# Optimization experiments

Measured on AMD Instinct MI355X. Metric: run time of the kernel, lower is better.

The kernel has to match this reference:

```python
import jax, jax.numpy as jnp
import numpy as np

N_NODES = 100000
N_EDGES = 3200000
NEG_SLOPE = 0.2  # PyG GATConv default
EPS = 1e-16      # PyG softmax denominator guard


def setup_inputs() -> dict:
    key = jax.random.key(0)
    ks = jax.random.split(key, 12)
    x = jax.random.normal(ks[0], (N_NODES, 4), dtype=jnp.float32)
    edge_index = jax.random.randint(ks[1], (2, N_EDGES), 0, N_NODES, dtype=jnp.int32)
    # conv1: in=4, heads=4, out=16, concat -> 64
    W1 = jax.random.normal(ks[2], (4, 64), dtype=jnp.float32) * 0.5
    a_src1 = jax.random.normal(ks[3], (4, 16), dtype=jnp.float32) * 0.3
    a_dst1 = jax.random.normal(ks[4], (4, 16), dtype=jnp.float32) * 0.3
    b1 = jnp.zeros((64,), dtype=jnp.float32)
    # conv2: in=64, heads=1, out=2, no concat
    W2 = jax.random.normal(ks[5], (64, 2), dtype=jnp.float32) * 0.2
    a_src2 = jax.random.normal(ks[6], (1, 2), dtype=jnp.float32) * 0.3
    a_dst2 = jax.random.normal(ks[7], (1, 2), dtype=jnp.float32) * 0.3
    b2 = jnp.zeros((2,), dtype=jnp.float32)
    return dict(x=x, edge_index=edge_index, W1=W1, a_src1=a_src1, a_dst1=a_dst1,
                b1=b1, W2=W2, a_src2=a_src2, a_dst2=a_dst2, b2=b2)


def _gat_layer(h_in, src, dst, W, a_s, a_d, b, heads, out_dim, concat):
    n = h_in.shape[0]
    h = (h_in @ W).reshape(n, heads, out_dim)            # [N, H, F]
    alpha_s = jnp.einsum('nhf,hf->nh', h, a_s)           # [N, H]
    alpha_d = jnp.einsum('nhf,hf->nh', h, a_d)
    e = jax.nn.leaky_relu(alpha_s[src] + alpha_d[dst], NEG_SLOPE)  # [E, H]
    # segment softmax over incoming edges of each dst node
    m = jax.ops.segment_max(e, dst, num_segments=n)      # [N, H]
    e = jnp.exp(e - m[dst])
    s = jax.ops.segment_sum(e, dst, num_segments=n)
    alpha = e / (s[dst] + EPS)                            # [E, H]
    msg = h[src] * alpha[:, :, None]                      # [E, H, F]
    out = jax.ops.segment_sum(msg, dst, num_segments=n)   # [N, H, F]
    if concat:
        out = out.reshape(n, heads * out_dim)
    else:
        out = out.mean(axis=1)
    return out + b


def reference(x, edge_index, W1, a_src1, a_dst1, b1, W2, a_src2, a_dst2, b2):
    n = x.shape[0]
    loop = jnp.arange(n, dtype=edge_index.dtype)
    src = jnp.concatenate([edge_index[0], loop])  # PyG add_self_loops=True
    dst = jnp.concatenate([edge_index[1], loop])
    h = jax.nn.elu(_gat_layer(x, src, dst, W1, a_src1, a_dst1, b1, 4, 16, True))
    h = _gat_layer(h, src, dst, W2, a_src2, a_dst2, b2, 1, 2, False)
    return jax.nn.log_softmax(h, axis=1)
```

## Files before the change

### kernel.cpp

```cpp
#include <hip/hip_runtime.h>
#include <hip/hip_fp16.h>
#include <math.h>

#define NEG_SLOPE 0.2f
#define EPS_F 1e-16f

#define P1_NB 256
#define P1S_THREADS 1024
#define LOCAL_BITS 7
#define NLOCAL 128
#define MAX_BEDGES 5632
#define REGS_PB 6
#define SCAN_SHIFT 11

__device__ __forceinline__ float leaky(float v) {
    return fmaxf(v, NEG_SLOPE * v);
}

__global__ void k_p1hist(const int* __restrict__ dst, int* __restrict__ histT,
                         int E, int chunk, int nbucket) {
    __shared__ int cnt[1024];
    int blk = blockIdx.x, t = threadIdx.x;
    for (int i = t; i < nbucket; i += P1S_THREADS) cnt[i] = 0;
    __syncthreads();
    int s = blk * chunk, e = min(E, s + chunk);
    for (int i = s + t; i < e; i += P1S_THREADS)
        atomicAdd(&cnt[dst[i] >> LOCAL_BITS], 1);
    __syncthreads();
    for (int i = t; i < nbucket; i += P1S_THREADS)
        histT[i * P1_NB + blk] = cnt[i];
}

__global__ void k_scan1(const int* __restrict__ in, int* __restrict__ out,
                        int* __restrict__ blockSums, int M) {
    __shared__ int sdata[256];
    int t = threadIdx.x;
    int base = blockIdx.x * 2048 + t * 8;
    int v[8];
    int total = 0;
#pragma unroll
    for (int k = 0; k < 8; ++k) {
        int idx = base + k;
        v[k] = (idx < M) ? in[idx] : 0;
        total += v[k];
    }
    sdata[t] = total;
    __syncthreads();
    for (int off = 1; off < 256; off <<= 1) {
        int x = (t >= off) ? sdata[t - off] : 0;
        __syncthreads();
        sdata[t] += x;
        __syncthreads();
    }
    int run = sdata[t] - total;
#pragma unroll
    for (int k = 0; k < 8; ++k) {
        int idx = base + k;
        if (idx < M) out[idx] = run;
        run += v[k];
    }
    if (t == 255) blockSums[blockIdx.x] = sdata[255];
}

__global__ void k_scan2(int* __restrict__ bs, int n) {
    __shared__ int s[128];
    int t = threadIdx.x;
    int v = (t < n) ? bs[t] : 0;
    s[t] = v;
    __syncthreads();
    for (int o = 1; o < 128; o <<= 1) {
        int x = (t >= o) ? s[t - o] : 0;
        __syncthreads();
        s[t] += x;
        __syncthreads();
    }
    if (t < n) bs[t] = s[t] - v;
}

__global__ void __launch_bounds__(1024)
k_scatterA(const int* __restrict__ src, const int* __restrict__ dst,
           const int* __restrict__ baseT, const int* __restrict__ bsScan,
           unsigned int* __restrict__ packed, int E, int chunk, int nbucket,
           const float* __restrict__ x, const float* __restrict__ W1,
           const float* __restrict__ a_src1, const float* __restrict__ a_dst1,
           __half* __restrict__ h1h, float* __restrict__ as1,
           float* __restrict__ ad1, int N) {
    __shared__ int cnt[1024];
    int blk = blockIdx.x, t = threadIdx.x;
    if (blk < P1_NB) {
        for (int i = t; i < nbucket; i += P1S_THREADS) {
            int idx = i * P1_NB + blk;
            cnt[i] = baseT[idx] + bsScan[idx >> SCAN_SHIFT];
        }
        __syncthreads();
        int s = blk * chunk, e = min(E, s + chunk);
        for (int i = s + t; i < e; i += P1S_THREADS) {
            int d = dst[i];
            int pos = atomicAdd(&cnt[d >> LOCAL_BITS], 1);
            packed[pos] = ((unsigned int)(d & (NLOCAL - 1)) << 23) | (unsigned int)src[i];
        }
    } else {
        int node = (blk - P1_NB) * 16 + (t >> 6);
        if (node >= N) return;
        int lane = t & 63;
        float4 xv = ((const float4*)x)[node];
        float h = xv.x * W1[lane] + xv.y * W1[64 + lane] +
                  xv.z * W1[128 + lane] + xv.w * W1[192 + lane];
        h1h[(size_t)node * 64 + lane] = __float2half(h);
        float as = h * a_src1[lane];
        float ad = h * a_dst1[lane];
#pragma unroll
        for (int m = 8; m >= 1; m >>= 1) {
            as += __shfl_xor(as, m, 16);
            ad += __shfl_xor(ad, m, 16);
        }
        if ((lane & 15) == 0) {
            int head = lane >> 4;
            as1[node * 4 + head] = as;
            ad1[node * 4 + head] = ad;
        }
    }
}

__global__ void k_fineL1(const unsigned int* __restrict__ packed, const int* __restrict__ baseT,
                         const int* __restrict__ bsScan,
                         const __half* __restrict__ h1h, const float* __restrict__ as1,
                         const float* __restrict__ ad1, const float* __restrict__ b1,
                         const float* __restrict__ W2, const float* __restrict__ a_src2,
                         const float* __restrict__ a_dst2,
                         int* __restrict__ csr, int* __restrict__ rowptr,
                         uint2* __restrict__ node2, int N, int E) {
    __shared__ int cnt[NLOCAL];
    __shared__ int off[NLOCAL];
    __shared__ int cur[NLOCAL];
    __shared__ unsigned int eb[MAX_BEDGES];

    int b = blockIdx.x, t = threadIdx.x;
    int nbucket = gridDim.x;
    int nodeBase = b << LOCAL_BITS;

    int i0 = b * P1_NB;
    int startE = baseT[i0] + bsScan[i0 >> SCAN_SHIFT];
    int endE = E;
    if (b != nbucket - 1) {
        int i1 = (b + 1) * P1_NB;
        endE = baseT[i1] + bsScan[i1 >> SCAN_SHIFT];
    }
    int ne = endE - startE;
    if (ne > MAX_BEDGES) ne = MAX_BEDGES;

    if (t < NLOCAL) cnt[t] = 0;
    __syncthreads();

    unsigned int pk[REGS_PB];
#pragma unroll
    for (int k = 0; k < REGS_PB; ++k) {
        int i = t + k * 1024;
        pk[k] = (i < ne) ? packed[startE + i] : 0xFFFFFFFFu;
    }
#pragma unroll
    for (int k = 0; k < REGS_PB; ++k)
        if (pk[k] != 0xFFFFFFFFu) atomicAdd(&cnt[pk[k] >> 23], 1);
    __syncthreads();
    if (t < NLOCAL) cur[t] = cnt[t];
    __syncthreads();
    for (int o = 1; o < NLOCAL; o <<= 1) {
        int v = (t < NLOCAL && t >= o) ? cur[t - o] : 0;
        __syncthreads();
        if (t < NLOCAL) cur[t] += v;
        __syncthreads();
    }
    if (t < NLOCAL) {
        int excl = cur[t] - cnt[t];
        off[t] = excl;
        int node = nodeBase + t;
        if (node < N) rowptr[node] = startE + excl;
    }
    if (b == 0 && t == 0) rowptr[N] = E;
    __syncthreads();
    if (t < NLOCAL) cur[t] = off[t];
    __syncthreads();
#pragma unroll
    for (int k = 0; k < REGS_PB; ++k)
        if (pk[k] != 0xFFFFFFFFu) {
            int pos = atomicAdd(&cur[pk[k] >> 23], 1);
            eb[pos] = pk[k];
        }
    __syncthreads();
    for (int i = t; i < ne; i += 1024)
        csr[startE + i] = (int)(eb[i] & 0x7FFFFFu);

    int wave = t >> 6;
    int lane = t & 63;
    int head4 = lane & 3;
    int j     = lane >> 2;
    int sub   = lane >> 4;
    int fl    = lane & 15;
    int h     = fl >> 2;

    for (int q = 0; q < 8; ++q) {
        int local = wave * 8 + q;
        int node = nodeBase + local;
        if (node >= N) break;
        int beg = off[local];
        int end = beg + cnt[local];

        float ad_s1 = ad1[node * 4 + head4];
        float pself4 = __expf(leaky(as1[node * 4 + head4] + ad_s1));
        float psum = (lane < 4) ? pself4 : 0.f;

        float pselfF = __shfl(pself4, h);
        float a0 = 0.f, a1 = 0.f, a2 = 0.f, a3 = 0.f;
        if (sub == 0) {
            float2 raw = *(const float2*)(h1h + ((size_t)node << 6) + (fl << 2));
            __half2 h01 = *reinterpret_cast<__half2*>(&raw.x);
            __half2 h23 = *reinterpret_cast<__half2*>(&raw.y);
            float2 f01 = __half22float2(h01), f23 = __half22float2(h23);
            a0 = pselfF * f01.x; a1 = pselfF * f01.y;
            a2 = pselfF * f23.x; a3 = pselfF * f23.y;
        }

        for (int c = beg; c < end; c += 16) {
            int e = c + j;
            bool valid = e < end;
            int s = (int)(eb[valid ? e : beg] & 0x7FFFFFu);
            float v = leaky(as1[s * 4 + head4] + ad_s1);
            float p = valid ? __expf(v) : 0.f;
            psum += p;

            int s_q[4];
#pragma unroll
            for (int m = 0; m < 4; ++m) s_q[m] = __shfl(s, m * 16 + sub * 4);
            float2 raw[4];
#pragma unroll
            for (int m = 0; m < 4; ++m)
                raw[m] = *(const float2*)(h1h + ((size_t)s_q[m] << 6) + (fl << 2));
            float p_q[4];
#pragma unroll
            for (int m = 0; m < 4; ++m) p_q[m] = __shfl(p, m * 16 + sub * 4 + h);
#pragma unroll
            for (int m = 0; m < 4; ++m) {
                __half2 h01 = *reinterpret_cast<__half2*>(&raw[m].x);
                __half2 h23 = *reinterpret_cast<__half2*>(&raw[m].y);
                float2 f01 = __half22float2(h01), f23 = __half22float2(h23);
                a0 = fmaf(p_q[m], f01.x, a0);
                a1 = fmaf(p_q[m], f01.y, a1);
                a2 = fmaf(p_q[m], f23.x, a2);
                a3 = fmaf(p_q[m], f23.y, a3);
            }
        }

        a0 += __shfl_xor(a0, 16); a0 += __shfl_xor(a0, 32);
        a1 += __shfl_xor(a1, 16); a1 += __shfl_xor(a1, 32);
        a2 += __shfl_xor(a2, 16); a2 += __shfl_xor(a2, 32);
        a3 += __shfl_xor(a3, 16); a3 += __shfl_xor(a3, 32);

#pragma unroll
        for (int m = 4; m <= 32; m <<= 1) psum += __shfl_xor(psum, m);
        float psumF = __shfl(psum, h);
        float inv = 1.f / (psumF + EPS_F);

        float4 b1v = ((const float4*)b1)[fl];
        float o0 = a0 * inv + b1v.x;
        float o1 = a1 * inv + b1v.y;
        float o2 = a2 * inv + b1v.z;
        float o3 = a3 * inv + b1v.w;
        float e0 = o0 > 0.f ? o0 : (__expf(o0) - 1.f);
        float e1 = o1 > 0.f ? o1 : (__expf(o1) - 1.f);
        float e2 = o2 > 0.f ? o2 : (__expf(o2) - 1.f);
        float e3 = o3 > 0.f ? o3 : (__expf(o3) - 1.f);

        float4 w01 = ((const float4*)W2)[fl * 2];
        float4 w23 = ((const float4*)W2)[fl * 2 + 1];
        float c0 = e0 * w01.x + e1 * w01.z + e2 * w23.x + e3 * w23.z;
        float c1 = e0 * w01.y + e1 * w01.w + e2 * w23.y + e3 * w23.w;
#pragma unroll
        for (int m = 8; m >= 1; m >>= 1) {
            c0 += __shfl_xor(c0, m);
            c1 += __shfl_xor(c1, m);
        }
        if (lane == 0) {
            float as2 = c0 * a_src2[0] + c1 * a_src2[1];
            float ad2 = c0 * a_dst2[0] + c1 * a_dst2[1];
            __half2 hc = __floats2half2_rn(c0, c1);
            __half2 ha = __floats2half2_rn(as2, ad2);
            node2[node] = make_uint2(*(unsigned int*)&hc, *(unsigned int*)&ha);
        }
    }
}

__global__ void k_layer2(const int* __restrict__ rowptr, const int* __restrict__ csr,
                         const uint2* __restrict__ node2, const float* __restrict__ b2,
                         float* __restrict__ out, int N) {
    int node = blockIdx.x * 16 + (threadIdx.x >> 4);
    if (node >= N) return;
    int sl = threadIdx.x & 15;

    uint2 mraw = node2[node];
    __half2 mch = *reinterpret_cast<__half2*>(&mraw.x);
    __half2 mah = *reinterpret_cast<__half2*>(&mraw.y);
    float2 mc = __half22float2(mch);
    float2 ma = __half22float2(mah);
    float ad = ma.y;
    int beg = rowptr[node], end = rowptr[node + 1];

    float psum = 0.f, a0 = 0.f, a1 = 0.f;
    for (int e = beg + sl; e < end; e += 16) {
        uint2 sraw = node2[csr[e]];
        __half2 sch = *reinterpret_cast<__half2*>(&sraw.x);
        __half2 sah = *reinterpret_cast<__half2*>(&sraw.y);
        float2 sc = __half22float2(sch);
        float2 sa = __half22float2(sah);
        float p = __expf(leaky(sa.x + ad));
        psum += p;
        a0 = fmaf(p, sc.x, a0);
        a1 = fmaf(p, sc.y, a1);
    }
    if (sl == 0) {
        float p = __expf(leaky(ma.x + ad));
        psum += p;
        a0 = fmaf(p, mc.x, a0);
        a1 = fmaf(p, mc.y, a1);
    }
#pragma unroll
    for (int m = 8; m >= 1; m >>= 1) {
        psum += __shfl_xor(psum, m);
        a0 += __shfl_xor(a0, m);
        a1 += __shfl_xor(a1, m);
    }
    if (sl == 0) {
        float inv = 1.f / (psum + EPS_F);
        float o0 = a0 * inv + b2[0];
        float o1 = a1 * inv + b2[1];
        float mx = fmaxf(o0, o1);
        float lse = mx + logf(__expf(o0 - mx) + __expf(o1 - mx));
        out[node * 2 + 0] = o0 - lse;
        out[node * 2 + 1] = o1 - lse;
    }
}


extern "C" void kernel_launch(void* const* d_in, const int* in_sizes, int n_in,
                              void* d_out, int out_size, void* d_ws, size_t ws_size,
                              hipStream_t stream) {
    const float* x      = (const float*)d_in[0];
    const int*   ei     = (const int*)d_in[1];
    const float* W1     = (const float*)d_in[2];
    const float* a_src1 = (const float*)d_in[3];
    const float* a_dst1 = (const float*)d_in[4];
    const float* b1     = (const float*)d_in[5];
    const float* W2     = (const float*)d_in[6];
    const float* a_src2 = (const float*)d_in[7];
    const float* a_dst2 = (const float*)d_in[8];
    const float* b2     = (const float*)d_in[9];
    float* out = (float*)d_out;

    int N = in_sizes[0] / 4;
    int E = in_sizes[1] / 2;
    const int* e_src = ei;
    const int* e_dst = ei + E;

    int nbucket = (N + NLOCAL - 1) >> LOCAL_BITS;
    int M = nbucket * P1_NB;

    char* w = (char*)d_ws;
    auto alloc = [&](size_t bytes) -> void* {
        void* p = (void*)w;
        w += (bytes + 255) & ~(size_t)255;
        return p;
    };
    __half* h1h       = (__half*)alloc((size_t)N * 64 * 2);
    float*  as1       = (float*)alloc((size_t)N * 4 * 4);
    float*  ad1       = (float*)alloc((size_t)N * 4 * 4);
    uint2*  node2     = (uint2*)alloc((size_t)N * 8);
    int*    rowptr    = (int*)alloc((size_t)(N + 1) * 4);
    int*    histT     = (int*)alloc((size_t)M * 4);
    int*    baseT     = (int*)alloc((size_t)M * 4);
    int*    blockSums = (int*)alloc(256 * 4);
    int*    csr       = (int*)alloc((size_t)E * 4);
    unsigned int* packed = (unsigned int*)alloc((size_t)E * 4);

    int chunk = (E + P1_NB - 1) / P1_NB;
    int nbScan = (M + 2047) / 2048;
    int nodeb16 = (N + 15) / 16;

    k_p1hist<<<P1_NB, P1S_THREADS, 0, stream>>>(e_dst, histT, E, chunk, nbucket);
    k_scan1<<<nbScan, 256, 0, stream>>>(histT, baseT, blockSums, M);
    k_scan2<<<1, 128, 0, stream>>>(blockSums, nbScan);
    k_scatterA<<<P1_NB + nodeb16, P1S_THREADS, 0, stream>>>(
        e_src, e_dst, baseT, blockSums, packed, E, chunk, nbucket,
        x, W1, a_src1, a_dst1, h1h, as1, ad1, N);
    k_fineL1<<<nbucket, 1024, 0, stream>>>(packed, baseT, blockSums,
                                           h1h, as1, ad1, b1, W2,
                                           a_src2, a_dst2, csr, rowptr, node2, N, E);
    k_layer2<<<nodeb16, 256, 0, stream>>>(rowptr, csr, node2, b2, out, N);
}
```

Before: 241.1 us.

## Fuse histogram, scan and scatter into one persistent kernel with grid barriers

Replaces the histogram, two-level scan and scatter kernels with a single 256-block kernel. It keeps each block's dst chunk in registers, accumulates per-bucket counts with global atomics, and synchronises the grid with atomic spin barriers. Block 0 then scans the bucket totals, and each block claims its offsets atomically before scattering the packed edges. Layer-1 node projection is folded in between the passes. This removes several launches and the reload of dst. In exchange, edge order within a bucket becomes nondeterministic, and the code relies on all 256 blocks being co-resident for the spin barrier to avoid deadlock.

```diff
diff --git a/kernel.cpp b/kernel.cpp
--- a/kernel.cpp
+++ b/kernel.cpp
@@ -5,125 +5,121 @@
 #define NEG_SLOPE 0.2f
 #define EPS_F 1e-16f
 
-#define P1_NB 256
-#define P1S_THREADS 1024
 #define LOCAL_BITS 7
 #define NLOCAL 128
 #define MAX_BEDGES 5632
 #define REGS_PB 6
-#define SCAN_SHIFT 11
+#define BUILD_NB 256
+#define DREGS 13
 
 __device__ __forceinline__ float leaky(float v) {
     return fmaxf(v, NEG_SLOPE * v);
 }
 
-__global__ void k_p1hist(const int* __restrict__ dst, int* __restrict__ histT,
-                         int E, int chunk, int nbucket) {
+__global__ void __launch_bounds__(1024, 4)
+k_build(const int* __restrict__ src, const int* __restrict__ dst,
+        int* __restrict__ ctrs, int* __restrict__ bucketBase, int* __restrict__ bucketCur,
+        unsigned int* __restrict__ packed, int E, int chunk, int nbucket,
+        const float* __restrict__ x, const float* __restrict__ W1,
+        const float* __restrict__ a_src1, const float* __restrict__ a_dst1,
+        __half* __restrict__ h1h, float* __restrict__ as1,
+        float* __restrict__ ad1, int N) {
     __shared__ int cnt[1024];
+    __shared__ int lcur[1024];
+
     int blk = blockIdx.x, t = threadIdx.x;
-    for (int i = t; i < nbucket; i += P1S_THREADS) cnt[i] = 0;
-    __syncthreads();
-    int s = blk * chunk, e = min(E, s + chunk);
-    for (int i = s + t; i < e; i += P1S_THREADS)
-        atomicAdd(&cnt[dst[i] >> LOCAL_BITS], 1);
-    __syncthreads();
-    for (int i = t; i < nbucket; i += P1S_THREADS)
-        histT[i * P1_NB + blk] = cnt[i];
-}
-
-__global__ void k_scan1(const int* __restrict__ in, int* __restrict__ out,
-                        int* __restrict__ blockSums, int M) {
-    __shared__ int sdata[256];
-    int t = threadIdx.x;
-    int base = blockIdx.x * 2048 + t * 8;
-    int v[8];
-    int total = 0;
-#pragma unroll
-    for (int k = 0; k < 8; ++k) {
-        int idx = base + k;
-        v[k] = (idx < M) ? in[idx] : 0;
-        total += v[k];
-    }
-    sdata[t] = total;
-    __syncthreads();
-    for (int off = 1; off < 256; off <<= 1) {
-        int x = (t >= off) ? sdata[t - off] : 0;
+    int* bucketCnt = ctrs;
+    int* barA = ctrs + 1024;
+    int* barB = ctrs + 1025;
+
+    cnt[t] = 0;
+    __syncthreads();
+
+    int s0 = blk * chunk, e0 = min(E, s0 + chunk);
+    int dreg[DREGS];
+#pragma unroll
+    for (int k = 0; k < DREGS; ++k) {
+        int i = s0 + t + k * 1024;
+        dreg[k] = (i < e0) ? dst[i] : -1;
+    }
+#pragma unroll
+    for (int k = 0; k < DREGS; ++k)
+        if (dreg[k] >= 0) atomicAdd(&cnt[dreg[k] >> LOCAL_BITS], 1);
+    __syncthreads();
+    if (t < nbucket && cnt[t] > 0) atomicAdd(&bucketCnt[t], cnt[t]);
+
+    {
+        int nspb = (N + BUILD_NB - 1) / BUILD_NB;
+        int base = blk * nspb, lim = min(N, base + nspb);
+        int lane = t & 63;
+        for (int node = base + (t >> 6); node < lim; node += 16) {
+            float4 xv = ((const float4*)x)[node];
+            float h = xv.x * W1[lane] + xv.y * W1[64 + lane] +
+                      xv.z * W1[128 + lane] + xv.w * W1[192 + lane];
+            h1h[(size_t)node * 64 + lane] = __float2half(h);
+            float as = h * a_src1[lane];
+            float ad = h * a_dst1[lane];
+#pragma unroll
+            for (int m = 8; m >= 1; m >>= 1) {
+                as += __shfl_xor(as, m, 16);
+                ad += __shfl_xor(ad, m, 16);
+            }
+            if ((lane & 15) == 0) {
+                as1[node * 4 + (lane >> 4)] = as;
+                ad1[node * 4 + (lane >> 4)] = ad;
+            }
+        }
+    }
+
+    __threadfence();
+    __syncthreads();
+    if (t == 0) {
+        atomicAdd(barA, 1);
+        while (atomicAdd(barA, 0) < (int)gridDim.x) __builtin_amdgcn_s_sleep(8);
+    }
+    __syncthreads();
+    __threadfence();
+
+    if (blk == 0) {
+        int v = (t < nbucket) ? bucketCnt[t] : 0;
+        lcur[t] = v;
         __syncthreads();
-        sdata[t] += x;
-        __syncthreads();
-    }
-    int run = sdata[t] - total;
-#pragma unroll
-    for (int k = 0; k < 8; ++k) {
-        int idx = base + k;
-        if (idx < M) out[idx] = run;
-        run += v[k];
-    }
-    if (t == 255) blockSums[blockIdx.x] = sdata[255];
-}
-
-__global__ void k_scan2(int* __restrict__ bs, int n) {
-    __shared__ int s[128];
-    int t = threadIdx.x;
-    int v = (t < n) ? bs[t] : 0;
-    s[t] = v;
-    __syncthreads();
-    for (int o = 1; o < 128; o <<= 1) {
-        int x = (t >= o) ? s[t - o] : 0;
-        __syncthreads();
-        s[t] += x;
-        __syncthreads();
-    }
-    if (t < n) bs[t] = s[t] - v;
-}
-
-__global__ void __launch_bounds__(1024)
-k_scatterA(const int* __restrict__ src, const int* __restrict__ dst,
-           const int* __restrict__ baseT, const int* __restrict__ bsScan,
-           unsigned int* __restrict__ packed, int E, int chunk, int nbucket,
-           const float* __restrict__ x, const float* __restrict__ W1,
-           const float* __restrict__ a_src1, const float* __restrict__ a_dst1,
-           __half* __restrict__ h1h, float* __restrict__ as1,
-           float* __restrict__ ad1, int N) {
-    __shared__ int cnt[1024];
-    int blk = blockIdx.x, t = threadIdx.x;
-    if (blk < P1_NB) {
-        for (int i = t; i < nbucket; i += P1S_THREADS) {
-            int idx = i * P1_NB + blk;
-            cnt[i] = baseT[idx] + bsScan[idx >> SCAN_SHIFT];
-        }
-        __syncthreads();
-        int s = blk * chunk, e = min(E, s + chunk);
-        for (int i = s + t; i < e; i += P1S_THREADS) {
-            int d = dst[i];
-            int pos = atomicAdd(&cnt[d >> LOCAL_BITS], 1);
-            packed[pos] = ((unsigned int)(d & (NLOCAL - 1)) << 23) | (unsigned int)src[i];
-        }
-    } else {
-        int node = (blk - P1_NB) * 16 + (t >> 6);
-        if (node >= N) return;
-        int lane = t & 63;
-        float4 xv = ((const float4*)x)[node];
-        float h = xv.x * W1[lane] + xv.y * W1[64 + lane] +
-                  xv.z * W1[128 + lane] + xv.w * W1[192 + lane];
-        h1h[(size_t)node * 64 + lane] = __float2half(h);
-        float as = h * a_src1[lane];
-        float ad = h * a_dst1[lane];
-#pragma unroll
-        for (int m = 8; m >= 1; m >>= 1) {
-            as += __shfl_xor(as, m, 16);
-            ad += __shfl_xor(ad, m, 16);
-        }
-        if ((lane & 15) == 0) {
-            int head = lane >> 4;
-            as1[node * 4 + head] = as;
-            ad1[node * 4 + head] = ad;
-        }
-    }
-}
-
-__global__ void k_fineL1(const unsigned int* __restrict__ packed, const int* __restrict__ baseT,
-                         const int* __restrict__ bsScan,
+        for (int o = 1; o < 1024; o <<= 1) {
+            int xv = (t >= o) ? lcur[t - o] : 0;
+            __syncthreads();
+            lcur[t] += xv;
+            __syncthreads();
+        }
+        int excl = lcur[t] - v;
+        if (t < nbucket) { bucketBase[t] = excl; bucketCur[t] = excl; }
+        if (t == 0) bucketBase[nbucket] = E;
+        __threadfence();
+    }
+
+    __syncthreads();
+    if (t == 0) {
+        atomicAdd(barB, 1);
+        while (atomicAdd(barB, 0) < (int)gridDim.x) __builtin_amdgcn_s_sleep(8);
+    }
+    __syncthreads();
+    __threadfence();
+
+    if (t < nbucket) lcur[t] = (cnt[t] > 0) ? atomicAdd(&bucketCur[t], cnt[t]) : 0;
+    __syncthreads();
+#pragma unroll
+    for (int k = 0; k < DREGS; ++k) {
+        int i = s0 + t + k * 1024;
+        if (i < e0) {
+            int d = dreg[k];
+            int sv = src[i];
+            int pos = atomicAdd(&lcur[d >> LOCAL_BITS], 1);
+            packed[pos] = ((unsigned int)(d & (NLOCAL - 1)) << 23) | (unsigned int)sv;
+        }
+    }
+}
+
+__global__ void k_fineL1(const unsigned int* __restrict__ packed,
+                         const int* __restrict__ bucketBase,
                          const __half* __restrict__ h1h, const float* __restrict__ as1,
                          const float* __restrict__ ad1, const float* __restrict__ b1,
                          const float* __restrict__ W2, const float* __restrict__ a_src2,
@@ -136,16 +132,10 @@
     __shared__ unsigned int eb[MAX_BEDGES];
 
     int b = blockIdx.x, t = threadIdx.x;
-    int nbucket = gridDim.x;
     int nodeBase = b << LOCAL_BITS;
 
-    int i0 = b * P1_NB;
-    int startE = baseT[i0] + bsScan[i0 >> SCAN_SHIFT];
-    int endE = E;
-    if (b != nbucket - 1) {
-        int i1 = (b + 1) * P1_NB;
-        endE = baseT[i1] + bsScan[i1 >> SCAN_SHIFT];
-    }
+    int startE = bucketBase[b];
+    int endE = bucketBase[b + 1];
     int ne = endE - startE;
     if (ne > MAX_BEDGES) ne = MAX_BEDGES;
 
@@ -361,7 +351,6 @@
     const int* e_dst = ei + E;
 
     int nbucket = (N + NLOCAL - 1) >> LOCAL_BITS;
-    int M = nbucket * P1_NB;
 
     char* w = (char*)d_ws;
     auto alloc = [&](size_t bytes) -> void* {
@@ -369,28 +358,25 @@
         w += (bytes + 255) & ~(size_t)255;
         return p;
     };
-    __half* h1h       = (__half*)alloc((size_t)N * 64 * 2);
-    float*  as1       = (float*)alloc((size_t)N * 4 * 4);
-    float*  ad1       = (float*)alloc((size_t)N * 4 * 4);
-    uint2*  node2     = (uint2*)alloc((size_t)N * 8);
-    int*    rowptr    = (int*)alloc((size_t)(N + 1) * 4);
-    int*    histT     = (int*)alloc((size_t)M * 4);
-    int*    baseT     = (int*)alloc((size_t)M * 4);
-    int*    blockSums = (int*)alloc(256 * 4);
-    int*    csr       = (int*)alloc((size_t)E * 4);
+    __half* h1h        = (__half*)alloc((size_t)N * 64 * 2);
+    float*  as1        = (float*)alloc((size_t)N * 4 * 4);
+    float*  ad1        = (float*)alloc((size_t)N * 4 * 4);
+    uint2*  node2      = (uint2*)alloc((size_t)N * 8);
+    int*    rowptr     = (int*)alloc((size_t)(N + 1) * 4);
+    int*    ctrs       = (int*)alloc(1026 * 4);
+    int*    bucketBase = (int*)alloc((size_t)(nbucket + 1) * 4);
+    int*    bucketCur  = (int*)alloc((size_t)nbucket * 4);
+    int*    csr        = (int*)alloc((size_t)E * 4);
     unsigned int* packed = (unsigned int*)alloc((size_t)E * 4);
 
-    int chunk = (E + P1_NB - 1) / P1_NB;
-    int nbScan = (M + 2047) / 2048;
+    int chunk = (E + BUILD_NB - 1) / BUILD_NB;
     int nodeb16 = (N + 15) / 16;
 
-    k_p1hist<<<P1_NB, P1S_THREADS, 0, stream>>>(e_dst, histT, E, chunk, nbucket);
-    k_scan1<<<nbScan, 256, 0, stream>>>(histT, baseT, blockSums, M);
-    k_scan2<<<1, 128, 0, stream>>>(blockSums, nbScan);
-    k_scatterA<<<P1_NB + nodeb16, P1S_THREADS, 0, stream>>>(
-        e_src, e_dst, baseT, blockSums, packed, E, chunk, nbucket,
-        x, W1, a_src1, a_dst1, h1h, as1, ad1, N);
-    k_fineL1<<<nbucket, 1024, 0, stream>>>(packed, baseT, blockSums,
+    hipMemsetAsync(ctrs, 0, 1026 * 4, stream);
+    k_build<<<BUILD_NB, 1024, 0, stream>>>(e_src, e_dst, ctrs, bucketBase, bucketCur,
+                                           packed, E, chunk, nbucket,
+                                           x, W1, a_src1, a_dst1, h1h, as1, ad1, N);
+    k_fineL1<<<nbucket, 1024, 0, stream>>>(packed, bucketBase,
                                            h1h, as1, ad1, b1, W2,
                                            a_src2, a_dst2, csr, rowptr, node2, N, E);
     k_layer2<<<nodeb16, 256, 0, stream>>>(rowptr, csr, node2, b2, out, N);
```

New measurement: 455.2 us. 1.89x slower.
